# Optimization experiments

Measured on AMD Instinct MI355X. Metric: run time of the kernel, lower is better.

## Reference

```python
import jax, jax.numpy as jnp
import numpy as np
from jax import lax

B, T, D, K = 2, 4096, 128, 256


def setup_inputs() -> dict:
    key = jax.random.key(0)
    ks = jax.random.split(key, 5)
    s = 0.05
    return {
        "z": jax.random.normal(ks[0], (B, T, D), jnp.float32),
        "conv_kernel": jax.random.normal(ks[1], (K, 1, D), jnp.float32) * s,  # flax WIO depthwise
        "conv_bias": jnp.zeros((D,), jnp.float32),
        "Wq": jax.random.normal(ks[2], (D, D), jnp.float32) * s,
        "bq": jnp.zeros((D,), jnp.float32),
        "Wk": jax.random.normal(ks[3], (D, D), jnp.float32) * s,
        "bk": jnp.zeros((D,), jnp.float32),
        "Wo": jax.random.normal(ks[4], (D, D), jnp.float32) * s,
        "bo": jnp.zeros((D,), jnp.float32),
    }


def _sphere_norm(x):
    return x / jnp.maximum(jnp.linalg.norm(x, axis=-1, keepdims=True), 1e-8)


def reference(z, conv_kernel, conv_bias, Wq, bq, Wk, bk, Wo, bo):
    Bv, Tv, Dv = z.shape
    Kv = conv_kernel.shape[0]

    # Depthwise causal memory conv (flax nn.Conv, padding='CAUSAL', groups=D)
    memory_force = lax.conv_general_dilated(
        z, conv_kernel, window_strides=(1,), padding=[(Kv - 1, 0)],
        dimension_numbers=("NWC", "WIO", "NWC"), feature_group_count=Dv,
    ) + conv_bias

    # Keys are computed from the base point z once, shared across RK4 stages
    k_hat = _sphere_norm(z @ Wk + bk)  # [B,T,D]
    mask = jnp.tril(jnp.ones((Tv, Tv), z.dtype))  # causal mask

    def vector_field(z_curr):
        q_hat = _sphere_norm(z_curr @ Wq + bq)
        dots = jnp.einsum("btd,bsd->bts", q_hat, k_hat)  # [B,T,T]
        attn = jnp.sin(dots) * mask  # Kuramoto-style sin coupling, causal
        kuramoto = jnp.einsum("bts,bsd->btd", attn, k_hat) @ Wo + bo
        total = memory_force + kuramoto
        # project to tangent space of the sphere at z_curr
        return total - jnp.sum(total * z_curr, axis=-1, keepdims=True) * z_curr

    h = 1.0

    def retract(z_base, v):
        return _sphere_norm(z_base + v)

    k1 = vector_field(z)
    k2 = vector_field(retract(z, 0.5 * h * k1))
    k3 = vector_field(retract(z, 0.5 * h * k2))
    k4 = vector_field(retract(z, h * k3))
    v_final = (h / 6.0) * (k1 + 2 * k2 + 2 * k3 + k4)
    return retract(z, v_final)
```

## Files before the change

### kernel.cpp

```cpp
#include <hip/hip_runtime.h>
#include <hip/hip_bf16.h>

#define BB 2
#define TT 4096
#define DD 128
#define KK 256
#define NROW (BB*TT)
#define NELT (NROW*DD)

typedef _Float16 f16;
typedef __attribute__((ext_vector_type(8))) f16 half8;
typedef __attribute__((ext_vector_type(2))) __fp16 fp16x2;
typedef __attribute__((ext_vector_type(4))) float f32x4;
typedef __attribute__((ext_vector_type(2))) int i32x2;

__device__ __forceinline__ int pack2(float a, float b){
  fp16x2 h = __builtin_amdgcn_cvt_pkrtz(a, b);
  return __builtin_bit_cast(int, h);
}

__global__ __launch_bounds__(256) void k_proj(
    const float* __restrict__ z, const float* __restrict__ Wk, const float* __restrict__ bk,
    f16* __restrict__ khb, f16* __restrict__ khT)
{
  __shared__ float Ws[DD*DD];
  __shared__ float zs[32*DD];
  int tid = threadIdx.x;
  int r0 = blockIdx.x * 32;
  #pragma unroll
  for (int it = 0; it < 16; it++){
    int idx = tid + it*256;
    *(f32x4*)(Ws + idx*4) = *(const f32x4*)(Wk + (size_t)idx*4);
  }
  #pragma unroll
  for (int it = 0; it < 4; it++){
    int idx = tid + it*256;
    *(f32x4*)(zs + idx*4) = *(const f32x4*)(z + (size_t)r0*DD + idx*4);
  }
  __syncthreads();
  int c = tid & 15, rr = tid >> 4;
  float acc0[8], acc1[8];
  #pragma unroll
  for (int u = 0; u < 8; u++){ float bv = bk[c*8+u]; acc0[u] = bv; acc1[u] = bv; }
  const float* zr0 = zs + rr*DD;
  const float* zr1 = zs + (rr+16)*DD;
  #pragma unroll 4
  for (int i = 0; i < DD; i++){
    f32x4 w0 = *(const f32x4*)(Ws + i*DD + c*8);
    f32x4 w1 = *(const f32x4*)(Ws + i*DD + c*8 + 4);
    float a0 = zr0[i], a1 = zr1[i];
    #pragma unroll
    for (int u = 0; u < 4; u++){
      acc0[u]   = fmaf(a0, w0[u], acc0[u]);   acc1[u]   = fmaf(a1, w0[u], acc1[u]);
      acc0[4+u] = fmaf(a0, w1[u], acc0[4+u]); acc1[4+u] = fmaf(a1, w1[u], acc1[4+u]);
    }
  }
  float s0 = 0.f, s1 = 0.f;
  #pragma unroll
  for (int u = 0; u < 8; u++){ s0 = fmaf(acc0[u], acc0[u], s0); s1 = fmaf(acc1[u], acc1[u], s1); }
  #pragma unroll
  for (int m = 1; m < 16; m <<= 1){ s0 += __shfl_xor(s0, m, 16); s1 += __shfl_xor(s1, m, 16); }
  float inv0 = 1.f / fmaxf(sqrtf(s0), 1e-8f);
  float inv1 = 1.f / fmaxf(sqrtf(s1), 1e-8f);
  half8 h0, h1;
  #pragma unroll
  for (int u = 0; u < 8; u++){ h0[u] = (f16)(acc0[u]*inv0); h1[u] = (f16)(acc1[u]*inv1); }
  int row0 = r0 + rr, row1 = row0 + 16;
  *(half8*)(khb + (size_t)row0*DD + c*8) = h0;
  *(half8*)(khb + (size_t)row1*DD + c*8) = h1;
  int b = row0 >> 12, t0 = row0 & 4095, t1 = row1 & 4095;
  #pragma unroll
  for (int u = 0; u < 8; u++){
    khT[((size_t)b*DD + c*8 + u)*TT + t0] = h0[u];
    khT[((size_t)b*DD + c*8 + u)*TT + t1] = h1[u];
  }
}

__global__ __launch_bounds__(256) void k_conv(
    const float* __restrict__ z, const float* __restrict__ ck, const float* __restrict__ cb,
    float* __restrict__ mf)
{
  int tid = threadIdx.x;
  int d = tid & 127, tg = tid >> 7;
  int bid = blockIdx.x;
  int b = bid >> 8;
  int tbase = ((bid & 255) << 4) + tg*8;
  const float* zb = z + (size_t)b*TT*DD;
  float acc[8];
  #pragma unroll
  for (int j = 0; j < 8; j++) acc[j] = 0.f;
  float ckq[8];
  #pragma unroll
  for (int u = 0; u < 8; u++) ckq[u] = 0.f;
  int sstart = tbase - (KK-1);
  for (int ch = 0; ch < 33; ch++){
    #pragma unroll
    for (int u = 0; u < 8; u++){
      int base = ch*8 + u;
      int s = sstart + base;
      float zv = ((unsigned)s < (unsigned)TT && base < 263) ? zb[(size_t)s*DD + d] : 0.f;
      ckq[u] = (base < KK) ? ck[(size_t)base*DD + d] : 0.f;
      #pragma unroll
      for (int j = 0; j < 8; j++) acc[j] = fmaf(ckq[(u-j)&7], zv, acc[j]);
    }
  }
  float cbv = cb[d];
  #pragma unroll
  for (int j = 0; j < 8; j++)
    mf[((size_t)b*TT + tbase + j)*DD + d] = acc[j] + cbv;
}

__global__ __launch_bounds__(256) void k_q(
    const float* __restrict__ zcur, const float* __restrict__ Wq, const float* __restrict__ bq,
    f16* __restrict__ qhb)
{
  __shared__ float Ws[DD*DD];
  __shared__ float zs[32*DD];
  int tid = threadIdx.x;
  int r0 = blockIdx.x * 32;
  #pragma unroll
  for (int it = 0; it < 16; it++){
    int idx = tid + it*256;
    *(f32x4*)(Ws + idx*4) = *(const f32x4*)(Wq + (size_t)idx*4);
  }
  #pragma unroll
  for (int it = 0; it < 4; it++){
    int idx = tid + it*256;
    *(f32x4*)(zs + idx*4) = *(const f32x4*)(zcur + (size_t)r0*DD + idx*4);
  }
  __syncthreads();
  int c = tid & 15, rr = tid >> 4;
  float acc0[8], acc1[8];
  #pragma unroll
  for (int u = 0; u < 8; u++){ float bv = bq[c*8+u]; acc0[u] = bv; acc1[u] = bv; }
  const float* zr0 = zs + rr*DD;
  const float* zr1 = zs + (rr+16)*DD;
  #pragma unroll 4
  for (int i = 0; i < DD; i++){
    f32x4 w0 = *(const f32x4*)(Ws + i*DD + c*8);
    f32x4 w1 = *(const f32x4*)(Ws + i*DD + c*8 + 4);
    float a0 = zr0[i], a1 = zr1[i];
    #pragma unroll
    for (int u = 0; u < 4; u++){
      acc0[u]   = fmaf(a0, w0[u], acc0[u]);   acc1[u]   = fmaf(a1, w0[u], acc1[u]);
      acc0[4+u] = fmaf(a0, w1[u], acc0[4+u]); acc1[4+u] = fmaf(a1, w1[u], acc1[4+u]);
    }
  }
  float s0 = 0.f, s1 = 0.f;
  #pragma unroll
  for (int u = 0; u < 8; u++){ s0 = fmaf(acc0[u], acc0[u], s0); s1 = fmaf(acc1[u], acc1[u], s1); }
  #pragma unroll
  for (int m = 1; m < 16; m <<= 1){ s0 += __shfl_xor(s0, m, 16); s1 += __shfl_xor(s1, m, 16); }
  float inv0 = 1.f / fmaxf(sqrtf(s0), 1e-8f);
  float inv1 = 1.f / fmaxf(sqrtf(s1), 1e-8f);
  half8 h0, h1;
  #pragma unroll
  for (int u = 0; u < 8; u++){ h0[u] = (f16)(acc0[u]*inv0); h1[u] = (f16)(acc1[u]*inv1); }
  *(half8*)(qhb + (size_t)(r0+rr)*DD + c*8) = h0;
  *(half8*)(qhb + (size_t)(r0+rr+16)*DD + c*8) = h1;
}

#define QTILE 128
#define NQT3 (TT/QTILE)
#define NCHUNK 272

__global__ __launch_bounds__(256,2) void k_attn9(
    const f16* __restrict__ qhb, const f16* __restrict__ khb,
    const f16* __restrict__ khT, f16* __restrict__ part)
{
  int bid = blockIdx.x;
  int b = bid / NCHUNK;
  int rem = bid - b*NCHUNK;
  int qt = 0, chunk = 0;
  #pragma unroll 1
  for (int j = 0; j < NQT3; j++){
    int nch = (j + 2) >> 1;
    if (rem < nch){ qt = j; chunk = rem; break; }
    rem -= nch;
  }
  int kt0 = chunk * 4;
  int kt1 = min(kt0 + 3, 2*qt + 1);
  int t0 = qt * QTILE;

  __shared__ __align__(16) f16 Kb[64*136];
  __shared__ __align__(16) f16 Kt[128*72];
  __shared__ __align__(16) f16 Ps[4][32*72];

  int tid  = threadIdx.x;
  int w    = tid >> 6;
  int lane = tid & 63;
  int n16  = lane & 15;
  int g    = lane >> 4;

  const f16* qg  = qhb + (size_t)b*TT*DD;
  const f16* kg  = khb + (size_t)b*TT*DD;
  const f16* ktg = khT + (size_t)b*DD*TT;

  int sb_r  = tid >> 4, sb_c = (tid & 15)*8;
  int st_r  = tid >> 3, st_c = (tid & 7)*8;

  half8 qa[2][4];
  #pragma unroll
  for (int p = 0; p < 2; p++){
    const f16* qrow = qg + (size_t)(t0 + 32*w + 16*p + n16)*DD + g*8;
    #pragma unroll
    for (int c = 0; c < 4; c++) qa[p][c] = *(const half8*)(qrow + 32*c);
  }
  f32x4 acc[2][8];
  #pragma unroll
  for (int p = 0; p < 2; p++)
    #pragma unroll
    for (int i = 0; i < 8; i++) acc[p][i] = (f32x4){0.f,0.f,0.f,0.f};

  f16* psw = &Ps[w][0];

  half8 sKb[4], sKt[4];
  {
    int s0 = kt0 * 64;
    #pragma unroll
    for (int it = 0; it < 4; it++)
      sKb[it] = *(const half8*)(kg + (size_t)(s0 + sb_r + it*16)*DD + sb_c);
    #pragma unroll
    for (int it = 0; it < 4; it++)
      sKt[it] = *(const half8*)(ktg + (size_t)(st_r + it*32)*TT + s0 + st_c);
  }

  for (int kt = kt0; kt <= kt1; kt++){
    #pragma unroll
    for (int it = 0; it < 4; it++)
      *(half8*)(Kb + (sb_r + it*16)*136 + sb_c) = sKb[it];
    #pragma unroll
    for (int it = 0; it < 4; it++)
      *(half8*)(Kt + (st_r + it*32)*72 + st_c) = sKt[it];
    __syncthreads();

    if (kt < kt1){
      int s0n = (kt+1) * 64;
      #pragma unroll
      for (int it = 0; it < 4; it++)
        sKb[it] = *(const half8*)(kg + (size_t)(s0n + sb_r + it*16)*DD + sb_c);
      #pragma unroll
      for (int it = 0; it < 4; it++)
        sKt[it] = *(const half8*)(ktg + (size_t)(st_r + it*32)*TT + s0n + st_c);
    }

    int s0 = kt * 64;
    f32x4 s_acc[2][4];
    #pragma unroll
    for (int p = 0; p < 2; p++)
      #pragma unroll
      for (int n = 0; n < 4; n++) s_acc[p][n] = (f32x4){0.f,0.f,0.f,0.f};
    #pragma unroll
    for (int c = 0; c < 4; c++){
      #pragma unroll
      for (int n = 0; n < 4; n++){
        half8 af = *(const half8*)(Kb + (16*n + n16)*136 + 32*c + g*8);
        s_acc[0][n] = __builtin_amdgcn_mfma_f32_16x16x32_f16(af, qa[0][c], s_acc[0][n], 0,0,0);
        s_acc[1][n] = __builtin_amdgcn_mfma_f32_16x16x32_f16(af, qa[1][c], s_acc[1][n], 0,0,0);
      }
    }
    #pragma unroll
    for (int p = 0; p < 2; p++){
      int qrow = t0 + 32*w + 16*p + n16;
      #pragma unroll
      for (int n = 0; n < 4; n++){
        int keyr = s0 + 16*n + 4*g;
        float v0 = (keyr     <= qrow) ? __sinf(s_acc[p][n][0]) : 0.f;
        float v1 = (keyr + 1 <= qrow) ? __sinf(s_acc[p][n][1]) : 0.f;
        float v2 = (keyr + 2 <= qrow) ? __sinf(s_acc[p][n][2]) : 0.f;
        float v3 = (keyr + 3 <= qrow) ? __sinf(s_acc[p][n][3]) : 0.f;
        i32x2 pw = { pack2(v0, v1), pack2(v2, v3) };
        *(i32x2*)(psw + (16*p + n16)*72 + 16*n + 4*g) = pw;
      }
    }

    #pragma unroll
    for (int h = 0; h < 2; h++){
      half8 pa[2];
      #pragma unroll
      for (int p = 0; p < 2; p++)
        pa[p] = *(const half8*)(psw + (16*p + n16)*72 + 32*h + 8*g);
      #pragma unroll
      for (int nt = 0; nt < 8; nt++){
        half8 bf = *(const half8*)(Kt + (16*nt + n16)*72 + 32*h + 8*g);
        acc[0][nt] = __builtin_amdgcn_mfma_f32_16x16x32_f16(pa[0], bf, acc[0][nt], 0,0,0);
        acc[1][nt] = __builtin_amdgcn_mfma_f32_16x16x32_f16(pa[1], bf, acc[1][nt], 0,0,0);
      }
    }
    __syncthreads();
  }

  f16* pb = part + (size_t)bid*(QTILE*DD) + (32*w)*DD;
  #pragma unroll
  for (int p = 0; p < 2; p++){
    #pragma unroll
    for (int nt = 0; nt < 8; nt++){
      #pragma unroll
      for (int r = 0; r < 4; r++){
        pb[(size_t)(16*p + 4*g + r)*DD + 16*nt + n16] = (f16)acc[p][nt][r];
      }
    }
  }
}

__global__ __launch_bounds__(256) void k_reduce(
    const f16* __restrict__ part, float* __restrict__ att)
{
  int bid = blockIdx.x;
  int rg = bid & 7;
  int qt = (bid >> 3) & 31;
  int b  = bid >> 8;
  int nc = (qt + 2) >> 1;
  int base = ((qt + 1)*(qt + 1)) >> 2;
  int tid = threadIdx.x;
  size_t off = (size_t)rg*(16*DD) + tid*8;
  const f16* src = part + ((size_t)b*NCHUNK + base)*(QTILE*DD) + off;
  float a[8];
  {
    half8 v = *(const half8*)(src);
    #pragma unroll
    for (int u = 0; u < 8; u++) a[u] = (float)v[u];
  }
  for (int c = 1; c < nc; c++){
    half8 v = *(const half8*)(src + (size_t)c*(QTILE*DD));
    #pragma unroll
    for (int u = 0; u < 8; u++) a[u] += (float)v[u];
  }
  float* dst = att + ((size_t)b*TT + (size_t)qt*QTILE)*DD + off;
  f32x4 o0 = {a[0],a[1],a[2],a[3]}, o1 = {a[4],a[5],a[6],a[7]};
  *(f32x4*)(dst) = o0;
  *(f32x4*)(dst + 4) = o1;
}

__global__ __launch_bounds__(256) void k_comb(
    const float* __restrict__ z, const float* __restrict__ Wo, const float* __restrict__ bo,
    const float* __restrict__ mf, const float* __restrict__ att,
    const float* __restrict__ zin, float* __restrict__ zout,
    float* __restrict__ vsum, float* __restrict__ out,
    float wsum, float cretr, int first, int last)
{
  __shared__ float Ws[DD*DD];
  __shared__ float As[32*DD];
  int tid = threadIdx.x;
  int r0 = blockIdx.x * 32;
  #pragma unroll
  for (int it = 0; it < 16; it++){
    int idx = tid + it*256;
    *(f32x4*)(Ws + idx*4) = *(const f32x4*)(Wo + (size_t)idx*4);
  }
  #pragma unroll
  for (int it = 0; it < 4; it++){
    int idx = tid + it*256;
    *(f32x4*)(As + idx*4) = *(const f32x4*)(att + (size_t)r0*DD + idx*4);
  }
  __syncthreads();
  int c = tid & 15, rr = tid >> 4;
  float kur0[8], kur1[8];
  #pragma unroll
  for (int u = 0; u < 8; u++){ float bv = bo[c*8+u]; kur0[u] = bv; kur1[u] = bv; }
  const float* ar0 = As + rr*DD;
  const float* ar1 = As + (rr+16)*DD;
  #pragma unroll 4
  for (int i = 0; i < DD; i++){
    f32x4 w0 = *(const f32x4*)(Ws + i*DD + c*8);
    f32x4 w1 = *(const f32x4*)(Ws + i*DD + c*8 + 4);
    float a0 = ar0[i], a1 = ar1[i];
    #pragma unroll
    for (int u = 0; u < 4; u++){
      kur0[u]   = fmaf(a0, w0[u], kur0[u]);   kur1[u]   = fmaf(a1, w0[u], kur1[u]);
      kur0[4+u] = fmaf(a0, w1[u], kur0[4+u]); kur1[4+u] = fmaf(a1, w1[u], kur1[4+u]);
    }
  }
  size_t o0 = (size_t)(r0+rr)*DD + c*8;
  size_t o1 = (size_t)(r0+rr+16)*DD + c*8;
  float tot0[8], tot1[8], zi0[8], zi1[8];
  {
    f32x4 m0a = *(const f32x4*)(mf + o0), m0b = *(const f32x4*)(mf + o0 + 4);
    f32x4 m1a = *(const f32x4*)(mf + o1), m1b = *(const f32x4*)(mf + o1 + 4);
    f32x4 z0a = *(const f32x4*)(zin + o0), z0b = *(const f32x4*)(zin + o0 + 4);
    f32x4 z1a = *(const f32x4*)(zin + o1), z1b = *(const f32x4*)(zin + o1 + 4);
    #pragma unroll
    for (int u = 0; u < 4; u++){
      tot0[u] = m0a[u] + kur0[u]; tot0[4+u] = m0b[u] + kur0[4+u];
      tot1[u] = m1a[u] + kur1[u]; tot1[4+u] = m1b[u] + kur1[4+u];
      zi0[u] = z0a[u]; zi0[4+u] = z0b[u];
      zi1[u] = z1a[u]; zi1[4+u] = z1b[u];
    }
  }
  float p0 = 0.f, p1 = 0.f;
  #pragma unroll
  for (int u = 0; u < 8; u++){ p0 = fmaf(tot0[u], zi0[u], p0); p1 = fmaf(tot1[u], zi1[u], p1); }
  #pragma unroll
  for (int m = 1; m < 16; m <<= 1){ p0 += __shfl_xor(p0, m, 16); p1 += __shfl_xor(p1, m, 16); }
  float ki0[8], ki1[8], vs0[8], vs1[8];
  #pragma unroll
  for (int u = 0; u < 8; u++){
    ki0[u] = tot0[u] - p0 * zi0[u];
    ki1[u] = tot1[u] - p1 * zi1[u];
  }
  if (first){
    #pragma unroll
    for (int u = 0; u < 8; u++){ vs0[u] = wsum*ki0[u]; vs1[u] = wsum*ki1[u]; }
  } else {
    f32x4 v0a = *(const f32x4*)(vsum + o0), v0b = *(const f32x4*)(vsum + o0 + 4);
    f32x4 v1a = *(const f32x4*)(vsum + o1), v1b = *(const f32x4*)(vsum + o1 + 4);
    #pragma unroll
    for (int u = 0; u < 4; u++){
      vs0[u] = fmaf(wsum, ki0[u], v0a[u]); vs0[4+u] = fmaf(wsum, ki0[4+u], v0b[u]);
      vs1[u] = fmaf(wsum, ki1[u], v1a[u]); vs1[4+u] = fmaf(wsum, ki1[4+u], v1b[u]);
    }
  }
  if (!last){
    f32x4 va = {vs0[0],vs0[1],vs0[2],vs0[3]}, vb = {vs0[4],vs0[5],vs0[6],vs0[7]};
    f32x4 vc = {vs1[0],vs1[1],vs1[2],vs1[3]}, vd = {vs1[4],vs1[5],vs1[6],vs1[7]};
    *(f32x4*)(vsum + o0) = va; *(f32x4*)(vsum + o0 + 4) = vb;
    *(f32x4*)(vsum + o1) = vc; *(f32x4*)(vsum + o1 + 4) = vd;
  }
  float nz0[8], nz1[8];
  {
    f32x4 z0a = *(const f32x4*)(z + o0), z0b = *(const f32x4*)(z + o0 + 4);
    f32x4 z1a = *(const f32x4*)(z + o1), z1b = *(const f32x4*)(z + o1 + 4);
    #pragma unroll
    for (int u = 0; u < 4; u++){
      float d0a = last ? vs0[u]*(1.f/6.f)   : cretr*ki0[u];
      float d0b = last ? vs0[4+u]*(1.f/6.f) : cretr*ki0[4+u];
      float d1a = last ? vs1[u]*(1.f/6.f)   : cretr*ki1[u];
      float d1b = last ? vs1[4+u]*(1.f/6.f) : cretr*ki1[4+u];
      nz0[u] = z0a[u] + d0a; nz0[4+u] = z0b[u] + d0b;
      nz1[u] = z1a[u] + d1a; nz1[4+u] = z1b[u] + d1b;
    }
  }
  float n0 = 0.f, n1 = 0.f;
  #pragma unroll
  for (int u = 0; u < 8; u++){ n0 = fmaf(nz0[u], nz0[u], n0); n1 = fmaf(nz1[u], nz1[u], n1); }
  #pragma unroll
  for (int m = 1; m < 16; m <<= 1){ n0 += __shfl_xor(n0, m, 16); n1 += __shfl_xor(n1, m, 16); }
  float i0 = 1.f / fmaxf(sqrtf(n0), 1e-8f);
  float i1 = 1.f / fmaxf(sqrtf(n1), 1e-8f);
  float* dst = last ? out : zout;
  f32x4 ra = {nz0[0]*i0, nz0[1]*i0, nz0[2]*i0, nz0[3]*i0};
  f32x4 rb = {nz0[4]*i0, nz0[5]*i0, nz0[6]*i0, nz0[7]*i0};
  f32x4 rc = {nz1[0]*i1, nz1[1]*i1, nz1[2]*i1, nz1[3]*i1};
  f32x4 rd = {nz1[4]*i1, nz1[5]*i1, nz1[6]*i1, nz1[7]*i1};
  *(f32x4*)(dst + o0) = ra; *(f32x4*)(dst + o0 + 4) = rb;
  *(f32x4*)(dst + o1) = rc; *(f32x4*)(dst + o1 + 4) = rd;
}

extern "C" void kernel_launch(void* const* d_in, const int* in_sizes, int n_in,
                              void* d_out, int out_size, void* d_ws, size_t ws_size,
                              hipStream_t stream) {
  const float* z  = (const float*)d_in[0];
  const float* ck = (const float*)d_in[1];
  const float* cb = (const float*)d_in[2];
  const float* Wq = (const float*)d_in[3];
  const float* bq = (const float*)d_in[4];
  const float* Wk = (const float*)d_in[5];
  const float* bk = (const float*)d_in[6];
  const float* Wo = (const float*)d_in[7];
  const float* bo = (const float*)d_in[8];
  float* out = (float*)d_out;

  float* mf   = (float*)d_ws;
  float* zc   = mf   + NELT;
  float* att  = zc   + NELT;
  float* vsum = att  + NELT;
  f16*   khb  = (f16*)(vsum + NELT);
  f16*   khT  = khb  + NELT;
  f16*   qhb  = khT  + NELT;
  f16*   part = qhb  + NELT;

  k_proj<<<NROW/32, 256, 0, stream>>>(z, Wk, bk, khb, khT);
  k_conv<<<BB*TT/16, 256, 0, stream>>>(z, ck, cb, mf);

  const float wv[4] = {1.f, 2.f, 2.f, 1.f};
  const float cv[4] = {0.5f, 0.5f, 1.f, 0.f};
  for (int st = 0; st < 4; st++){
    const float* zcur = (st == 0) ? z : zc;
    k_q     <<<NROW/32, 256, 0, stream>>>(zcur, Wq, bq, qhb);
    k_attn9 <<<BB*NCHUNK, 256, 0, stream>>>(qhb, khb, khT, part);
    k_reduce<<<BB*NQT3*8, 256, 0, stream>>>(part, att);
    k_comb  <<<NROW/32, 256, 0, stream>>>(z, Wo, bo, mf, att, zcur, zc, vsum, out,
                                          wv[st], cv[st], st == 0, st == 3);
  }
}
```

Measured before the change: 309.3 us.

## Load attention K operands directly from global memory instead of LDS staging

The attention kernel no longer stages K and K-transpose tiles through shared memory with register prefetch and block barriers. Each wave now reads its MFMA operand fragments straight from global memory, relying on L1/L2 caching, since all four waves read the same K tiles. This removes the LDS stores and both __syncthreads per key tile and frees LDS. In exchange, each wave issues redundant global loads with no software prefetch, so the MFMAs may stall on global latency.

```diff
diff --git a/kernel.cpp b/kernel.cpp
--- a/kernel.cpp
+++ b/kernel.cpp
@@ -164,7 +164,7 @@
 #define NQT3 (TT/QTILE)
 #define NCHUNK 272
 
-__global__ __launch_bounds__(256,2) void k_attn9(
+__global__ __launch_bounds__(256,2) void k_attn10(
     const f16* __restrict__ qhb, const f16* __restrict__ khb,
     const f16* __restrict__ khT, f16* __restrict__ part)
 {
@@ -182,8 +182,6 @@
   int kt1 = min(kt0 + 3, 2*qt + 1);
   int t0 = qt * QTILE;
 
-  __shared__ __align__(16) f16 Kb[64*136];
-  __shared__ __align__(16) f16 Kt[128*72];
   __shared__ __align__(16) f16 Ps[4][32*72];
 
   int tid  = threadIdx.x;
@@ -196,9 +194,6 @@
   const f16* kg  = khb + (size_t)b*TT*DD;
   const f16* ktg = khT + (size_t)b*DD*TT;
 
-  int sb_r  = tid >> 4, sb_c = (tid & 15)*8;
-  int st_r  = tid >> 3, st_c = (tid & 7)*8;
-
   half8 qa[2][4];
   #pragma unroll
   for (int p = 0; p < 2; p++){
@@ -213,37 +208,10 @@
     for (int i = 0; i < 8; i++) acc[p][i] = (f32x4){0.f,0.f,0.f,0.f};
 
   f16* psw = &Ps[w][0];
-
-  half8 sKb[4], sKt[4];
-  {
-    int s0 = kt0 * 64;
-    #pragma unroll
-    for (int it = 0; it < 4; it++)
-      sKb[it] = *(const half8*)(kg + (size_t)(s0 + sb_r + it*16)*DD + sb_c);
-    #pragma unroll
-    for (int it = 0; it < 4; it++)
-      sKt[it] = *(const half8*)(ktg + (size_t)(st_r + it*32)*TT + s0 + st_c);
-  }
+  const f16* kArow = kg  + (size_t)n16*DD + g*8;
+  const f16* kBrow = ktg + (size_t)n16*TT + g*8;
 
   for (int kt = kt0; kt <= kt1; kt++){
-    #pragma unroll
-    for (int it = 0; it < 4; it++)
-      *(half8*)(Kb + (sb_r + it*16)*136 + sb_c) = sKb[it];
-    #pragma unroll
-    for (int it = 0; it < 4; it++)
-      *(half8*)(Kt + (st_r + it*32)*72 + st_c) = sKt[it];
-    __syncthreads();
-
-    if (kt < kt1){
-      int s0n = (kt+1) * 64;
-      #pragma unroll
-      for (int it = 0; it < 4; it++)
-        sKb[it] = *(const half8*)(kg + (size_t)(s0n + sb_r + it*16)*DD + sb_c);
-      #pragma unroll
-      for (int it = 0; it < 4; it++)
-        sKt[it] = *(const half8*)(ktg + (size_t)(st_r + it*32)*TT + s0n + st_c);
-    }
-
     int s0 = kt * 64;
     f32x4 s_acc[2][4];
     #pragma unroll
@@ -254,7 +222,7 @@
     for (int c = 0; c < 4; c++){
       #pragma unroll
       for (int n = 0; n < 4; n++){
-        half8 af = *(const half8*)(Kb + (16*n + n16)*136 + 32*c + g*8);
+        half8 af = *(const half8*)(kArow + (size_t)(s0 + 16*n)*DD + 32*c);
         s_acc[0][n] = __builtin_amdgcn_mfma_f32_16x16x32_f16(af, qa[0][c], s_acc[0][n], 0,0,0);
         s_acc[1][n] = __builtin_amdgcn_mfma_f32_16x16x32_f16(af, qa[1][c], s_acc[1][n], 0,0,0);
       }
@@ -282,12 +250,11 @@
         pa[p] = *(const half8*)(psw + (16*p + n16)*72 + 32*h + 8*g);
       #pragma unroll
       for (int nt = 0; nt < 8; nt++){
-        half8 bf = *(const half8*)(Kt + (16*nt + n16)*72 + 32*h + 8*g);
+        half8 bf = *(const half8*)(kBrow + (size_t)(16*nt)*TT + s0 + 32*h);
         acc[0][nt] = __builtin_amdgcn_mfma_f32_16x16x32_f16(pa[0], bf, acc[0][nt], 0,0,0);
         acc[1][nt] = __builtin_amdgcn_mfma_f32_16x16x32_f16(pa[1], bf, acc[1][nt], 0,0,0);
       }
     }
-    __syncthreads();
   }
 
   f16* pb = part + (size_t)bid*(QTILE*DD) + (32*w)*DD;
@@ -477,7 +444,7 @@
   for (int st = 0; st < 4; st++){
     const float* zcur = (st == 0) ? z : zc;
     k_q     <<<NROW/32, 256, 0, stream>>>(zcur, Wq, bq, qhb);
-    k_attn9 <<<BB*NCHUNK, 256, 0, stream>>>(qhb, khb, khT, part);
+    k_attn10<<<BB*NCHUNK, 256, 0, stream>>>(qhb, khb, khT, part);
     k_reduce<<<BB*NQT3*8, 256, 0, stream>>>(part, att);
     k_comb  <<<NROW/32, 256, 0, stream>>>(z, Wo, bo, mf, att, zcur, zc, vsum, out,
                                           wv[st], cv[st], st == 0, st == 3);
```

Result: slower. 413.6 us (+33.7%).
